# Performance work log

Hardware: AMD Instinct MI355X
Metric: run time of the kernel (lower is better)

Reference implementation:

```python
import jax, jax.numpy as jnp
import numpy as np

BN_EPS = 1e-5

def setup_inputs() -> dict:
    key = jax.random.key(0)
    ks = jax.random.split(key, 6)
    N, C, T, V = 64, 64, 300, 25
    Ci, Co, S = 16, 64, 3  # inter_channels = out//4, num_subset = 3
    x = jax.random.normal(ks[0], (N, C, T, V), dtype=jnp.float32)
    # static (non-trainable) adjacency buffer; graph_attn is init.constant_(1)
    A_static = jax.random.uniform(ks[1], (S, V, V), dtype=jnp.float32)
    graph_attn = jnp.ones((S, V, V), jnp.float32)
    # stacked 1x1 conv weights for the 3 subsets: (S, out_c, in_c)
    Wg = jax.random.normal(ks[2], (S, Co, C), jnp.float32) * 0.05
    bg = jnp.zeros((S, Co), jnp.float32)
    Wa = jax.random.normal(ks[3], (S, Ci, C), jnp.float32) * 0.05
    ba = jnp.zeros((S, Ci), jnp.float32)
    Wb = jax.random.normal(ks[4], (S, Ci, C), jnp.float32) * 0.05
    bb = jnp.zeros((S, Ci), jnp.float32)
    # BatchNorm2d (eval mode: running stats)
    gamma = jnp.ones((Co,), jnp.float32)
    beta = jnp.zeros((Co,), jnp.float32)
    run_mean = jnp.zeros((Co,), jnp.float32)
    run_var = jnp.ones((Co,), jnp.float32)
    return {"x": x, "A_static": A_static, "graph_attn": graph_attn,
            "Wg": Wg, "bg": bg, "Wa": Wa, "ba": ba, "Wb": Wb, "bb": bb,
            "gamma": gamma, "beta": beta, "run_mean": run_mean, "run_var": run_var}

def _conv1x1(x, W, b):
    # x: (N,C,T,V), W: (O,C), b: (O,) -> (N,O,T,V)
    return jnp.einsum('nctv,oc->notv', x, W) + b[None, :, None, None]

def reference(x, A_static, graph_attn, Wg, bg, Wa, ba, Wb, bb, gamma, beta, run_mean, run_var):
    N, C, T, V = x.shape
    Ci = Wa.shape[1]
    A = A_static + graph_attn            # (3, V, V)
    x_flat = x.reshape(N, C * T, V)
    hidden = jnp.zeros((), x.dtype)
    for i in range(Wg.shape[0]):
        a = _conv1x1(x, Wa[i], ba[i])                                  # (N,Ci,T,V)
        b2 = _conv1x1(x, Wb[i], bb[i])                                 # (N,Ci,T,V)
        A1 = a.transpose(0, 3, 1, 2).reshape(N, V, Ci * T)             # (N,V,Ci*T)
        A2 = b2.reshape(N, Ci * T, V)                                  # (N,Ci*T,V)
        attn = jax.nn.softmax(jnp.matmul(A1, A2) / (Ci * T), axis=-2)  # softmax over dim -2
        attn = attn + A[i]                                             # (N,V,V)
        y = jnp.matmul(x_flat, attn).reshape(N, C, T, V)
        hidden = hidden + _conv1x1(y, Wg[i], bg[i])
    inv = (gamma / jnp.sqrt(run_var + BN_EPS))[None, :, None, None]
    hn = (hidden - run_mean[None, :, None, None]) * inv + beta[None, :, None, None]
    return jax.nn.relu(hn + x)  # in_channels == out_channels -> identity residual
```

## Files before the change

kernel.cpp:

```cpp
#include <hip/hip_runtime.h>

typedef unsigned short u16;
typedef __attribute__((ext_vector_type(8))) short short8;
typedef __attribute__((ext_vector_type(4))) float float4v;

#define TVB 7500
#define CTVB 480000

union U8S { short8 s; uint4 u; };

static __device__ __forceinline__ u16 f2bfc(float f) {
    union { float f; unsigned u; } x; x.f = f;
    return (u16)((x.u + 0x8000u) >> 16);
}
static __device__ __forceinline__ unsigned pk2(float a, float b) {
    union { float f; unsigned u; } xa, xb; xa.f = a; xb.f = b;
    return __builtin_amdgcn_perm(xb.u + 0x8000u, xa.u + 0x8000u, 0x07060302u);
}

__global__ __launch_bounds__(256, 3) void kA(
    const float* __restrict__ xg, const float* __restrict__ Wa, const float* __restrict__ ba,
    const float* __restrict__ Wb, const float* __restrict__ bb, float* __restrict__ Sws)
{
    __shared__ u16 xT[4][32][72];
    __shared__ u16 asT[3][32][72];
    __shared__ u16 bsT[3][32][72];
    const int tid  = threadIdx.x;
    const int lane = tid & 63;
    const int w    = tid >> 6;
    const int l15  = lane & 15;
    const int q    = lane >> 4;
    const int n    = blockIdx.y;
    const int t0   = blockIdx.x * 12;

    for (int e = tid; e < 4 * 7 * 72; e += 256) {
        int tt = e / 504;
        int r  = e - tt * 504;
        xT[tt][25 + r / 72][r % 72] = 0;
    }

    short8 waf[2], wbf[2];
    float ba_r[4], bb_r[4];
    if (w < 3) {
        #pragma unroll
        for (int kf = 0; kf < 2; ++kf) {
            const float* pa = Wa + w * 1024 + l15 * 64 + kf * 32 + q * 8;
            const float* pb = Wb + w * 1024 + l15 * 64 + kf * 32 + q * 8;
            float4 a0 = *(const float4*)pa, a1 = *(const float4*)(pa + 4);
            float4 b0 = *(const float4*)pb, b1 = *(const float4*)(pb + 4);
            U8S ta, tb;
            ta.u = make_uint4(pk2(a0.x, a0.y), pk2(a0.z, a0.w), pk2(a1.x, a1.y), pk2(a1.z, a1.w));
            tb.u = make_uint4(pk2(b0.x, b0.y), pk2(b0.z, b0.w), pk2(b1.x, b1.y), pk2(b1.z, b1.w));
            waf[kf] = ta.s; wbf[kf] = tb.s;
        }
        #pragma unroll
        for (int r = 0; r < 4; ++r) {
            ba_r[r] = ba[w * 16 + q * 4 + r];
            bb_r[r] = bb[w * 16 + q * 4 + r];
        }
    }

    float4v accS[3];
    #pragma unroll
    for (int i = 0; i < 3; ++i) accS[i] = (float4v){0.f, 0.f, 0.f, 0.f};

    const float* xb = xg + (size_t)n * CTVB;

    for (int g = 0; g < 3; ++g) {
        __syncthreads();
        const float* xs = xb + (t0 + g * 4) * 25;
        #pragma unroll 2
        for (int e = tid; e < 3200; e += 256) {
            int c = e / 50;
            int p = e - c * 50;
            int j = 2 * p;
            float2 v2 = *(const float2*)(xs + c * TVB + j);
            int tt0 = j / 25, u0 = j - tt0 * 25;
            int j1 = j + 1;
            int tt1 = j1 / 25, u1 = j1 - tt1 * 25;
            xT[tt0][u0][c] = f2bfc(v2.x);
            xT[tt1][u1][c] = f2bfc(v2.y);
        }
        __syncthreads();
        if (w < 3) {
            #pragma unroll
            for (int tt = 0; tt < 4; ++tt) {
                float4v aA0 = {0,0,0,0}, aA1 = {0,0,0,0}, aB0 = {0,0,0,0}, aB1 = {0,0,0,0};
                #pragma unroll
                for (int kf = 0; kf < 2; ++kf) {
                    short8 x0 = *(const short8*)&xT[tt][l15][kf * 32 + q * 8];
                    short8 x1 = *(const short8*)&xT[tt][16 + l15][kf * 32 + q * 8];
                    aA0 = __builtin_amdgcn_mfma_f32_16x16x32_bf16(waf[kf], x0, aA0, 0, 0, 0);
                    aA1 = __builtin_amdgcn_mfma_f32_16x16x32_bf16(waf[kf], x1, aA1, 0, 0, 0);
                    aB0 = __builtin_amdgcn_mfma_f32_16x16x32_bf16(wbf[kf], x0, aB0, 0, 0, 0);
                    aB1 = __builtin_amdgcn_mfma_f32_16x16x32_bf16(wbf[kf], x1, aB1, 0, 0, 0);
                }
                int kb = tt * 16 + q * 4;
                uint2 ua0 = { pk2(aA0[0] + ba_r[0], aA0[1] + ba_r[1]), pk2(aA0[2] + ba_r[2], aA0[3] + ba_r[3]) };
                uint2 ua1 = { pk2(aA1[0] + ba_r[0], aA1[1] + ba_r[1]), pk2(aA1[2] + ba_r[2], aA1[3] + ba_r[3]) };
                uint2 ub0 = { pk2(aB0[0] + bb_r[0], aB0[1] + bb_r[1]), pk2(aB0[2] + bb_r[2], aB0[3] + bb_r[3]) };
                uint2 ub1 = { pk2(aB1[0] + bb_r[0], aB1[1] + bb_r[1]), pk2(aB1[2] + bb_r[2], aB1[3] + bb_r[3]) };
                *(uint2*)&asT[w][l15][kb]      = ua0;
                *(uint2*)&asT[w][16 + l15][kb] = ua1;
                *(uint2*)&bsT[w][l15][kb]      = ub0;
                *(uint2*)&bsT[w][16 + l15][kb] = ub1;
            }
        }
        __syncthreads();
        const int mt = w >> 1, nt = w & 1;
        #pragma unroll
        for (int i = 0; i < 3; ++i) {
            #pragma unroll
            for (int ks = 0; ks < 2; ++ks) {
                short8 af  = *(const short8*)&asT[i][mt * 16 + l15][ks * 32 + q * 8];
                short8 bf_ = *(const short8*)&bsT[i][nt * 16 + l15][ks * 32 + q * 8];
                accS[i] = __builtin_amdgcn_mfma_f32_16x16x32_bf16(af, bf_, accS[i], 0, 0, 0);
            }
        }
    }
    const int mt = w >> 1, nt = w & 1;
    #pragma unroll
    for (int i = 0; i < 3; ++i) {
        #pragma unroll
        for (int r = 0; r < 4; ++r) {
            int u = mt * 16 + q * 4 + r;
            int v = nt * 16 + l15;
            if (u < 25 && v < 25)
                atomicAdd(&Sws[(i * 64 + n) * 625 + u * 25 + v], accS[i][r]);
        }
    }
}

__global__ __launch_bounds__(64) void kS(float* __restrict__ Sws,
    const float* __restrict__ Ast, const float* __restrict__ Gat)
{
    int g = blockIdx.x;
    int i = g >> 6;
    int v = threadIdx.x;
    if (v >= 25) return;
    float vals[25];
    float m = -1e30f;
    #pragma unroll
    for (int u = 0; u < 25; ++u) {
        float s = Sws[g * 625 + u * 25 + v] * (1.0f / 4800.0f);
        vals[u] = s;
        m = fmaxf(m, s);
    }
    float sum = 0.f;
    #pragma unroll
    for (int u = 0; u < 25; ++u) { float e = __expf(vals[u] - m); vals[u] = e; sum += e; }
    float isum = 1.f / sum;
    #pragma unroll
    for (int u = 0; u < 25; ++u) {
        int idx = i * 625 + u * 25 + v;
        Sws[g * 625 + u * 25 + v] = vals[u] * isum + Ast[idx] + Gat[idx];
    }
}

__global__ __launch_bounds__(256, 4) void kB(
    const float* __restrict__ xg, const float* __restrict__ Wgp, const float* __restrict__ bgp,
    const float* __restrict__ gam, const float* __restrict__ bet, const float* __restrict__ rmu,
    const float* __restrict__ rva, const float* __restrict__ attnw, float* __restrict__ outg)
{
    __shared__ u16 xsu[3][64][32];
    __shared__ u16 ysT[32][200];
    __shared__ u16 pTs[3][32][40];
    const int tid  = threadIdx.x;
    const int lane = tid & 63;
    const int w    = tid >> 6;
    const int l15  = lane & 15;
    const int q    = lane >> 4;
    const int n    = blockIdx.y;
    const int t0   = blockIdx.x * 3;

    for (int e = tid; e < 3 * 32 * 40; e += 256) ((u16*)pTs)[e] = 0;
    const float* xb = xg + (size_t)n * CTVB;
    #pragma unroll 2
    for (int e = tid; e < 64 * 38; e += 256) {
        int c = e / 38;
        int p = e - c * 38;
        const float* src = xb + c * TVB + t0 * 25;
        if (p < 37) {
            int j = 2 * p;
            float2 v2 = *(const float2*)(src + j);
            int tt0 = j / 25, u0 = j - tt0 * 25;
            int j1 = j + 1;
            int tt1 = j1 / 25, u1 = j1 - tt1 * 25;
            xsu[tt0][c][u0] = f2bfc(v2.x);
            xsu[tt1][c][u1] = f2bfc(v2.y);
        } else {
            xsu[2][c][24] = f2bfc(src[74]);
        }
    }
    for (int e = tid; e < 3 * 64 * 7; e += 256) {
        int tt = e / 448;
        int r  = e - tt * 448;
        xsu[tt][r / 7][25 + r % 7] = 0;
    }
    for (int e = tid; e < 1875; e += 256) {
        int i = e / 625;
        int r = e - i * 625;
        int u = r / 25;
        int v = r - u * 25;
        pTs[i][v][u] = f2bfc(attnw[(i * 64 + n) * 625 + r]);
    }

    short8 wgf[6];
    #pragma unroll
    for (int kf = 0; kf < 6; ++kf) {
        int i  = kf >> 1;
        int c0 = (kf & 1) * 32 + q * 8;
        const float* p = Wgp + i * 4096 + (w * 16 + l15) * 64 + c0;
        float4 f0 = *(const float4*)p, f1 = *(const float4*)(p + 4);
        U8S t;
        t.u = make_uint4(pk2(f0.x, f0.y), pk2(f0.z, f0.w), pk2(f1.x, f1.y), pk2(f1.z, f1.w));
        wgf[kf] = t.s;
    }
    float invr[4], add0r[4];
    #pragma unroll
    for (int r = 0; r < 4; ++r) {
        int o = w * 16 + q * 4 + r;
        float gv = gam[o], bt = bet[o], mu = rmu[o], vv = rva[o];
        float bgs = bgp[o] + bgp[64 + o] + bgp[128 + o];
        float iv = gv * rsqrtf(vv + 1e-5f);
        invr[r] = iv;
        add0r[r] = (bgs - mu) * iv + bt;
    }
    __syncthreads();
    short8 pf[3][2];
    #pragma unroll
    for (int i = 0; i < 3; ++i)
        #pragma unroll
        for (int nt = 0; nt < 2; ++nt)
            pf[i][nt] = *(const short8*)&pTs[i][nt * 16 + l15][q * 8];

    #pragma unroll
    for (int tl = 0; tl < 3; ++tl) {
        short8 xf = *(const short8*)&xsu[tl][w * 16 + l15][q * 8];
        #pragma unroll
        for (int i = 0; i < 3; ++i) {
            #pragma unroll
            for (int nt = 0; nt < 2; ++nt) {
                float4v acc = {0, 0, 0, 0};
                acc = __builtin_amdgcn_mfma_f32_16x16x32_bf16(xf, pf[i][nt], acc, 0, 0, 0);
                uint2 pk = { pk2(acc[0], acc[1]), pk2(acc[2], acc[3]) };
                *(uint2*)&ysT[nt * 16 + l15][i * 64 + w * 16 + q * 4] = pk;
            }
        }
        __syncthreads();
        #pragma unroll
        for (int nt = 0; nt < 2; ++nt) {
            float4v acc = {0, 0, 0, 0};
            #pragma unroll
            for (int kf = 0; kf < 6; ++kf) {
                short8 yf = *(const short8*)&ysT[nt * 16 + l15][kf * 32 + q * 8];
                acc = __builtin_amdgcn_mfma_f32_16x16x32_bf16(wgf[kf], yf, acc, 0, 0, 0);
            }
            int v = nt * 16 + l15;
            if (v < 25) {
                int base_o = w * 16 + q * 4;
                const float* xrp = xb + (size_t)base_o * TVB + (t0 + tl) * 25 + v;
                float* op = outg + (size_t)n * CTVB + (size_t)base_o * TVB + (t0 + tl) * 25 + v;
                #pragma unroll
                for (int r = 0; r < 4; ++r) {
                    float xres = xrp[(size_t)r * TVB];
                    float val = fmaf(acc[r], invr[r], add0r[r]) + xres;
                    op[(size_t)r * TVB] = fmaxf(val, 0.f);
                }
            }
        }
        __syncthreads();
    }
}

extern "C" void kernel_launch(void* const* d_in, const int* in_sizes, int n_in,
                              void* d_out, int out_size, void* d_ws, size_t ws_size,
                              hipStream_t stream) {
    const float* x    = (const float*)d_in[0];
    const float* Ast  = (const float*)d_in[1];
    const float* Gat  = (const float*)d_in[2];
    const float* Wg   = (const float*)d_in[3];
    const float* bg   = (const float*)d_in[4];
    const float* Wa   = (const float*)d_in[5];
    const float* ba   = (const float*)d_in[6];
    const float* Wb   = (const float*)d_in[7];
    const float* bb   = (const float*)d_in[8];
    const float* gam  = (const float*)d_in[9];
    const float* bet  = (const float*)d_in[10];
    const float* rmu  = (const float*)d_in[11];
    const float* rva  = (const float*)d_in[12];
    float* out = (float*)d_out;
    float* Sws = (float*)d_ws;

    hipMemsetAsync(Sws, 0, 192 * 625 * sizeof(float), stream);
    kA<<<dim3(25, 64), 256, 0, stream>>>(x, Wa, ba, Wb, bb, Sws);
    kS<<<dim3(192), 64, 0, stream>>>(Sws, Ast, Gat);
    kB<<<dim3(100, 64), 256, 0, stream>>>(x, Wg, bg, gam, bet, rmu, rva, Sws, out);
}
```

Baseline: 410.9 us.

## Replace atomic score accumulation with partial buffers and reuse shared x for residual

kA now writes per-time-block partial attention scores into a scratch area (aliased onto the output buffer) instead of atomically adding, removing the memset and atomic contention; kS reduces the 25 partials before the softmax. kB takes the residual from the bf16 x tile already in shared memory rather than re-reading fp32 x from global. This trades extra partial-buffer traffic for no atomics, and the residual now carries bf16 rounding error.

```diff
diff --git a/kernel.cpp b/kernel.cpp
--- a/kernel.cpp
+++ b/kernel.cpp
@@ -9,6 +9,9 @@
 
 union U8S { short8 s; uint4 u; };
 
+static __device__ __forceinline__ float bf2f(u16 a) {
+    union { unsigned u; float f; } x; x.u = ((unsigned)a) << 16; return x.f;
+}
 static __device__ __forceinline__ u16 f2bfc(float f) {
     union { float f; unsigned u; } x; x.f = f;
     return (u16)((x.u + 0x8000u) >> 16);
@@ -20,7 +23,7 @@
 
 __global__ __launch_bounds__(256, 3) void kA(
     const float* __restrict__ xg, const float* __restrict__ Wa, const float* __restrict__ ba,
-    const float* __restrict__ Wb, const float* __restrict__ bb, float* __restrict__ Sws)
+    const float* __restrict__ Wb, const float* __restrict__ bb, float* __restrict__ part)
 {
     __shared__ u16 xT[4][32][72];
     __shared__ u16 asT[3][32][72];
@@ -119,6 +122,7 @@
         }
     }
     const int mt = w >> 1, nt = w & 1;
+    const size_t pbase = ((size_t)blockIdx.x * 64 + n) * 3;
     #pragma unroll
     for (int i = 0; i < 3; ++i) {
         #pragma unroll
@@ -126,34 +130,46 @@
             int u = mt * 16 + q * 4 + r;
             int v = nt * 16 + l15;
             if (u < 25 && v < 25)
-                atomicAdd(&Sws[(i * 64 + n) * 625 + u * 25 + v], accS[i][r]);
-        }
-    }
-}
-
-__global__ __launch_bounds__(64) void kS(float* __restrict__ Sws,
+                part[(pbase + i) * 625 + u * 25 + v] = accS[i][r];
+        }
+    }
+}
+
+__global__ __launch_bounds__(256) void kS(const float* __restrict__ part, float* __restrict__ Sws,
     const float* __restrict__ Ast, const float* __restrict__ Gat)
 {
-    int g = blockIdx.x;
-    int i = g >> 6;
-    int v = threadIdx.x;
-    if (v >= 25) return;
-    float vals[25];
-    float m = -1e30f;
-    #pragma unroll
-    for (int u = 0; u < 25; ++u) {
-        float s = Sws[g * 625 + u * 25 + v] * (1.0f / 4800.0f);
-        vals[u] = s;
-        m = fmaxf(m, s);
-    }
-    float sum = 0.f;
-    #pragma unroll
-    for (int u = 0; u < 25; ++u) { float e = __expf(vals[u] - m); vals[u] = e; sum += e; }
-    float isum = 1.f / sum;
-    #pragma unroll
-    for (int u = 0; u < 25; ++u) {
-        int idx = i * 625 + u * 25 + v;
-        Sws[g * 625 + u * 25 + v] = vals[u] * isum + Ast[idx] + Gat[idx];
+    __shared__ float ssum[625];
+    const int g = blockIdx.x;
+    const int i = g >> 6;
+    const int n = g & 63;
+    const int tid = threadIdx.x;
+    for (int e = tid; e < 625; e += 256) {
+        float s = 0.f;
+        #pragma unroll 5
+        for (int tb = 0; tb < 25; ++tb)
+            s += part[(((size_t)tb * 64 + n) * 3 + i) * 625 + e];
+        ssum[e] = s;
+    }
+    __syncthreads();
+    if (tid < 25) {
+        const int v = tid;
+        float vals[25];
+        float m = -1e30f;
+        #pragma unroll
+        for (int u = 0; u < 25; ++u) {
+            float s = ssum[u * 25 + v] * (1.0f / 4800.0f);
+            vals[u] = s;
+            m = fmaxf(m, s);
+        }
+        float sum = 0.f;
+        #pragma unroll
+        for (int u = 0; u < 25; ++u) { float e = __expf(vals[u] - m); vals[u] = e; sum += e; }
+        float isum = 1.f / sum;
+        #pragma unroll
+        for (int u = 0; u < 25; ++u) {
+            int idx = i * 625 + u * 25 + v;
+            Sws[g * 625 + u * 25 + v] = vals[u] * isum + Ast[idx] + Gat[idx];
+        }
     }
 }
 
@@ -259,11 +275,11 @@
             int v = nt * 16 + l15;
             if (v < 25) {
                 int base_o = w * 16 + q * 4;
-                const float* xrp = xb + (size_t)base_o * TVB + (t0 + tl) * 25 + v;
                 float* op = outg + (size_t)n * CTVB + (size_t)base_o * TVB + (t0 + tl) * 25 + v;
                 #pragma unroll
                 for (int r = 0; r < 4; ++r) {
-                    float xres = xrp[(size_t)r * TVB];
+                    int o = base_o + r;
+                    float xres = bf2f(xsu[tl][o][v]);
                     float val = fmaf(acc[r], invr[r], add0r[r]) + xres;
                     op[(size_t)r * TVB] = fmaxf(val, 0.f);
                 }
@@ -289,11 +305,11 @@
     const float* bet  = (const float*)d_in[10];
     const float* rmu  = (const float*)d_in[11];
     const float* rva  = (const float*)d_in[12];
-    float* out = (float*)d_out;
-    float* Sws = (float*)d_ws;
-
-    hipMemsetAsync(Sws, 0, 192 * 625 * sizeof(float), stream);
-    kA<<<dim3(25, 64), 256, 0, stream>>>(x, Wa, ba, Wb, bb, Sws);
-    kS<<<dim3(192), 64, 0, stream>>>(Sws, Ast, Gat);
+    float* out  = (float*)d_out;
+    float* Sws  = (float*)d_ws;
+    float* part = out;
+
+    kA<<<dim3(25, 64), 256, 0, stream>>>(x, Wa, ba, Wb, bb, part);
+    kS<<<dim3(192), 256, 0, stream>>>(part, Sws, Ast, Gat);
     kB<<<dim3(100, 64), 256, 0, stream>>>(x, Wg, bg, gam, bet, rmu, rva, Sws, out);
 }
```

Measured after the change: 389.9 us. 1.05x faster.
